# Kernel optimization log

Hardware: AMD Instinct MI355X
Metric: run time of the kernel (lower is better)

The kernel has to match this reference:

```python
import jax, jax.numpy as jnp
import numpy as np

N_QUBITS = 12
FAST_DEPTH = 4
FAST_DECAY = 0.9
LATENT = 512
BATCH = 2048


def _apply_ry(state, theta, wire):
    # state: (B, 2**n) real; RY is a real rotation. PennyLane default.qubit:
    # wire 0 is the most-significant bit of the state index.
    B = state.shape[0]
    s = state.reshape(B, 1 << wire, 2, -1)
    h = theta * 0.5
    c = jnp.cos(h)[:, None, None]
    sn = jnp.sin(h)[:, None, None]
    s0, s1 = s[:, :, 0], s[:, :, 1]
    out = jnp.stack([c * s0 - sn * s1, sn * s0 + c * s1], axis=2)
    return out.reshape(state.shape)


def _apply_cnot_adjacent(state, wire):
    # CNOT with control=wire, target=wire+1 (nearest-neighbor chain)
    B = state.shape[0]
    s = state.reshape(B, 1 << wire, 2, 2, -1)
    out = jnp.stack([s[:, :, 0], s[:, :, 1, ::-1]], axis=2)
    return out.reshape(state.shape)


def _fwp_circuit(x, fast, n_qubits, n_outputs):
    # x: (B, n_qubits) RY encoding angles; fast: (B, depth, n_qubits)
    B = x.shape[0]
    dim = 1 << n_qubits
    # Hadamard layer on |0...0> -> uniform positive real amplitudes.
    state = jnp.full((B, dim), 2.0 ** (-n_qubits / 2), dtype=x.dtype)
    for w in range(n_qubits):
        state = _apply_ry(state, x[:, w], w)
    for layer in range(fast.shape[1]):
        for w in range(n_qubits - 1):
            state = _apply_cnot_adjacent(state, w)
        for w in range(n_qubits):
            state = _apply_ry(state, fast[:, layer, w], w)
    probs = state * state  # real state -> |amp|^2
    outs = []
    for w in range(n_outputs):
        p = probs.reshape(B, 1 << w, 2, -1)
        outs.append(p[:, :, 0].sum(axis=(1, 2)) - p[:, :, 1].sum(axis=(1, 2)))
    return jnp.stack(outs, axis=1)  # (B, n_outputs) PauliZ expvals


def setup_inputs() -> dict:
    key = jax.random.key(0)
    ks = jax.random.split(key, 6)
    n, depth, latent = N_QUBITS, FAST_DEPTH, LATENT
    return {
        "x_t": jax.random.normal(ks[0], (BATCH, n), jnp.float32),
        "fast_prev": jax.random.normal(ks[1], (BATCH, depth, n), jnp.float32) * 0.1,
        "W_enc": jax.random.normal(ks[2], (latent, n), jnp.float32) / np.sqrt(n).astype(np.float32),
        "b_enc": jnp.zeros((latent,), jnp.float32),
        "W_upd": jax.random.normal(ks[3], (depth * n, latent), jnp.float32) / np.sqrt(latent).astype(np.float32),
        "b_upd": jnp.zeros((depth * n,), jnp.float32),
        "W_ro": jax.random.normal(ks[4], (1, n), jnp.float32) / np.sqrt(n).astype(np.float32),
        "b_ro": jnp.zeros((1,), jnp.float32),
    }


def reference(x_t, fast_prev, W_enc, b_enc, W_upd, b_upd, W_ro, b_ro):
    latent = jnp.tanh(x_t @ W_enc.T + b_enc)
    delta = (latent @ W_upd.T + b_upd).reshape(x_t.shape[0], FAST_DEPTH, N_QUBITS)
    fast_next = FAST_DECAY * fast_prev + delta
    q_out = _fwp_circuit(x_t, fast_next, N_QUBITS, N_QUBITS)  # n_outputs = n_qubits
    y_t = q_out @ W_ro.T + b_ro
    return (y_t, fast_next)
```

## Files before the change

### kernel.cpp

```cpp
#include <hip/hip_runtime.h>

static constexpr int NQ    = 12;
static constexpr int DEPTH = 4;
static constexpr int LAT   = 512;
static constexpr int FAST  = DEPTH * NQ;
static constexpr float DECAY = 0.9f;
static constexpr int PITCH = 66;

using v2f = __attribute__((ext_vector_type(2))) float;


#define RAW_FENCE() __threadfence_block()
#define WAR_FENCE() __builtin_amdgcn_wave_barrier()

template<int S>
__device__ __forceinline__ void bfly2(float (&v)[64], float c, float s) {
    v2f c2 = {c, c}, s2 = {s, s};
    #pragma unroll
    for (int r0 = 0; r0 < 64; r0 += 2) {
        if ((r0 & S) == 0) {
            v2f a = {v[r0],     v[r0 + 1]};
            v2f b = {v[r0 + S], v[r0 + S + 1]};
            v2f na = c2 * a - s2 * b;
            v2f nb = s2 * a + c2 * b;
            v[r0]         = na.x;  v[r0 + 1]     = na.y;
            v[r0 + S]     = nb.x;  v[r0 + S + 1] = nb.y;
        }
    }
}

__device__ __forceinline__ void bfly1(float (&v)[64], float c, float s) {
    v2f cs = {c, s}, nsc = {-s, c};
    #pragma unroll
    for (int r0 = 0; r0 < 64; r0 += 2) {
        float a = v[r0], b = v[r0 + 1];
        v2f aa = {a, a}, bb = {b, b};
        v2f res = cs * aa + nsc * bb;
        v[r0]     = res.x;
        v[r0 + 1] = res.y;
    }
}

__device__ __forceinline__ void ry6(float (&v)[64], const float* lc, const float* ls) {
    bfly2<32>(v, lc[0], ls[0]);
    bfly2<16>(v, lc[1], ls[1]);
    bfly2<8>(v, lc[2], ls[2]);
    bfly2<4>(v, lc[3], ls[3]);
    bfly2<2>(v, lc[4], ls[4]);
    bfly1(v, lc[5], ls[5]);
}

__global__ __launch_bounds__(64, 2)
void fwp_kernel(const float* __restrict__ x_t,
                const float* __restrict__ fast_prev,
                const float* __restrict__ W_enc,
                const float* __restrict__ b_enc,
                const float* __restrict__ W_upd,
                const float* __restrict__ b_upd,
                const float* __restrict__ W_ro,
                const float* __restrict__ b_ro,
                float* __restrict__ out_y,
                float* __restrict__ out_fast) {
    const int lane = threadIdx.x;
    const int b    = blockIdx.x;

    __shared__ __align__(16) float s_xch[64 * PITCH];
    __shared__ float s_c[FAST], s_s[FAST];

    float* s_lat = s_xch;

    float xr = (lane < NQ) ? x_t[b * NQ + lane] : 0.0f;
    float xa[NQ];
    #pragma unroll
    for (int k = 0; k < NQ; k++) xa[k] = __shfl(xr, k, 64);

    #pragma unroll
    for (int t = 0; t < LAT / 64; t++) {
        int j = lane + 64 * t;
        const float4* wr = (const float4*)(W_enc + j * NQ);
        float4 a0 = wr[0], a1 = wr[1], a2 = wr[2];
        float sum = b_enc[j]
            + a0.x * xa[0] + a0.y * xa[1] + a0.z * xa[2]  + a0.w * xa[3]
            + a1.x * xa[4] + a1.y * xa[5] + a1.z * xa[6]  + a1.w * xa[7]
            + a2.x * xa[8] + a2.y * xa[9] + a2.z * xa[10] + a2.w * xa[11];
        s_lat[j] = tanhf(sum);
    }
    RAW_FENCE();

    if (lane < FAST) {
        const float4* wr = (const float4*)(W_upd + lane * LAT);
        const float4* lr = (const float4*)(s_lat);
        float sum = b_upd[lane];
        #pragma unroll 16
        for (int j = 0; j < LAT / 4; j++) {
            float4 w4 = wr[j];
            float4 l4 = lr[j];
            sum += w4.x * l4.x + w4.y * l4.y + w4.z * l4.z + w4.w * l4.w;
        }
        float ang = DECAY * fast_prev[b * FAST + lane] + sum;
        out_fast[b * FAST + lane] = ang;
        float hh = 0.5f * ang;
        s_c[lane] = __cosf(hh);
        s_s[lane] = __sinf(hh);
    }
    RAW_FENCE();

    float g0[NQ], g1[NQ];
    #pragma unroll
    for (int w = 0; w < NQ; w++) {
        float hh = 0.5f * xa[w];
        float c = __cosf(hh), s = __sinf(hh);
        g0[w] = (c - s) * 0.70710678118654752f;
        g1[w] = (c + s) * 0.70710678118654752f;
    }
    float L = 1.0f;
    #pragma unroll
    for (int w = 0; w < 6; w++)
        L *= ((lane >> (5 - w)) & 1) ? g1[w] : g0[w];

    float v[64];
    v[0] = L;
    #pragma unroll
    for (int w = 6; w < NQ; w++) {
        const int S = 1 << (11 - w);
        #pragma unroll
        for (int r = 0; r < 64; r += 2 * S) {
            v[r + S] = v[r] * g1[w];
            v[r]     = v[r] * g0[w];
        }
    }

    const int A0 = ((lane ^ (lane >> 1)) & 31) | (lane & 32);
    const int A1 = A0 ^ 32;

    #pragma unroll
    for (int layer = 0; layer < DEPTH; layer++) {
        float lc[NQ], ls[NQ];
        #pragma unroll
        for (int w = 0; w < NQ; w++) {
            lc[w] = s_c[layer * NQ + w];
            ls[w] = s_s[layer * NQ + w];
        }

        WAR_FENCE();
        #pragma unroll
        for (int k = 0; k < 32; k++)
            *(v2f*)&s_xch[lane * PITCH + 2 * k] = (v2f){v[2 * k], v[2 * k + 1]};
        RAW_FENCE();
        #pragma unroll
        for (int r = 0; r < 64; r++) {
            const int g = r ^ (r >> 1);
            v[r] = s_xch[g * PITCH + ((r & 1) ? A1 : A0)];
        }
        ry6(v, lc, ls);

        WAR_FENCE();
        #pragma unroll
        for (int k = 0; k < 32; k++)
            *(v2f*)&s_xch[lane * PITCH + 2 * k] = (v2f){v[2 * k], v[2 * k + 1]};
        RAW_FENCE();
        #pragma unroll
        for (int r = 0; r < 64; r++) v[r] = s_xch[r * PITCH + lane];
        ry6(v, lc + 6, ls + 6);
    }

    float tot = 0.0f, pw[6] = {0, 0, 0, 0, 0, 0};
    #pragma unroll
    for (int r = 0; r < 64; r++) {
        float p = v[r] * v[r];
        tot += p;
        pw[0] += (r & 32) ? -p : p;
        pw[1] += (r & 16) ? -p : p;
        pw[2] += (r & 8)  ? -p : p;
        pw[3] += (r & 4)  ? -p : p;
        pw[4] += (r & 2)  ? -p : p;
        pw[5] += (r & 1)  ? -p : p;
    }
    float sl = 0.0f;
    #pragma unroll
    for (int w = 0; w < 6; w++) {
        float c = W_ro[w];
        sl += ((lane >> (5 - w)) & 1) ? -c : c;
    }
    float y = sl * tot;
    #pragma unroll
    for (int k = 0; k < 6; k++) y += W_ro[6 + k] * pw[k];
    #pragma unroll
    for (int m = 32; m >= 1; m >>= 1) y += __shfl_xor(y, m, 64);
    if (lane == 0) out_y[b] = y + b_ro[0];
}

extern "C" void kernel_launch(void* const* d_in, const int* in_sizes, int n_in,
                              void* d_out, int out_size, void* d_ws, size_t ws_size,
                              hipStream_t stream) {
    const float* x_t       = (const float*)d_in[0];
    const float* fast_prev = (const float*)d_in[1];
    const float* W_enc     = (const float*)d_in[2];
    const float* b_enc     = (const float*)d_in[3];
    const float* W_upd     = (const float*)d_in[4];
    const float* b_upd     = (const float*)d_in[5];
    const float* W_ro      = (const float*)d_in[6];
    const float* b_ro      = (const float*)d_in[7];
    float* out = (float*)d_out;

    fwp_kernel<<<2048, 64, 0, stream>>>(x_t, fast_prev, W_enc, b_enc,
                                        W_upd, b_upd, W_ro, b_ro,
                                        out , out + 2048 );
}
```

Measured before the change: 111.3 us.

## Split butterfly stages into halves to overlap LDS reads and drop fences

Each 6-wire RY block becomes two 5-wire butterfly passes over the 32-element halves plus a final stride-32 butterfly. The second half of the LDS transpose reads can then be issued while the first half is still being rotated. All block fences and wave barriers around the shared-memory exchange are removed, since the block is a single 64-lane wavefront. The x row is also read directly from global memory by every lane instead of being broadcast with shuffles. Without fences, correct ordering of the LDS exchange now depends on the compiler not reordering accesses across lanes.

```diff
diff --git a/kernel.cpp b/kernel.cpp
--- a/kernel.cpp
+++ b/kernel.cpp
@@ -10,14 +10,11 @@
 using v2f = __attribute__((ext_vector_type(2))) float;
 
 
-#define RAW_FENCE() __threadfence_block()
-#define WAR_FENCE() __builtin_amdgcn_wave_barrier()
-
-template<int S>
-__device__ __forceinline__ void bfly2(float (&v)[64], float c, float s) {
+template<int S, int B>
+__device__ __forceinline__ void bfly_half(float (&v)[64], float c, float s) {
     v2f c2 = {c, c}, s2 = {s, s};
     #pragma unroll
-    for (int r0 = 0; r0 < 64; r0 += 2) {
+    for (int r0 = B; r0 < B + 32; r0 += 2) {
         if ((r0 & S) == 0) {
             v2f a = {v[r0],     v[r0 + 1]};
             v2f b = {v[r0 + S], v[r0 + S + 1]};
@@ -29,10 +26,11 @@
     }
 }
 
-__device__ __forceinline__ void bfly1(float (&v)[64], float c, float s) {
+template<int B>
+__device__ __forceinline__ void bfly1_half(float (&v)[64], float c, float s) {
     v2f cs = {c, s}, nsc = {-s, c};
     #pragma unroll
-    for (int r0 = 0; r0 < 64; r0 += 2) {
+    for (int r0 = B; r0 < B + 32; r0 += 2) {
         float a = v[r0], b = v[r0 + 1];
         v2f aa = {a, a}, bb = {b, b};
         v2f res = cs * aa + nsc * bb;
@@ -41,13 +39,26 @@
     }
 }
 
-__device__ __forceinline__ void ry6(float (&v)[64], const float* lc, const float* ls) {
-    bfly2<32>(v, lc[0], ls[0]);
-    bfly2<16>(v, lc[1], ls[1]);
-    bfly2<8>(v, lc[2], ls[2]);
-    bfly2<4>(v, lc[3], ls[3]);
-    bfly2<2>(v, lc[4], ls[4]);
-    bfly1(v, lc[5], ls[5]);
+template<int B>
+__device__ __forceinline__ void ry5_half(float (&v)[64], const float* c, const float* s) {
+    bfly_half<16, B>(v, c[0], s[0]);
+    bfly_half<8,  B>(v, c[1], s[1]);
+    bfly_half<4,  B>(v, c[2], s[2]);
+    bfly_half<2,  B>(v, c[3], s[3]);
+    bfly1_half<B>(v, c[4], s[4]);
+}
+
+__device__ __forceinline__ void bfly32(float (&v)[64], float c, float s) {
+    v2f c2 = {c, c}, s2 = {s, s};
+    #pragma unroll
+    for (int r0 = 0; r0 < 32; r0 += 2) {
+        v2f a = {v[r0],      v[r0 + 1]};
+        v2f b = {v[r0 + 32], v[r0 + 33]};
+        v2f na = c2 * a - s2 * b;
+        v2f nb = s2 * a + c2 * b;
+        v[r0]      = na.x;  v[r0 + 1]  = na.y;
+        v[r0 + 32] = nb.x;  v[r0 + 33] = nb.y;
+    }
 }
 
 __global__ __launch_bounds__(64, 2)
@@ -69,10 +80,10 @@
 
     float* s_lat = s_xch;
 
-    float xr = (lane < NQ) ? x_t[b * NQ + lane] : 0.0f;
+    const float* xrow = x_t + b * NQ;
     float xa[NQ];
     #pragma unroll
-    for (int k = 0; k < NQ; k++) xa[k] = __shfl(xr, k, 64);
+    for (int k = 0; k < NQ; k++) xa[k] = xrow[k];
 
     #pragma unroll
     for (int t = 0; t < LAT / 64; t++) {
@@ -85,7 +96,6 @@
             + a2.x * xa[8] + a2.y * xa[9] + a2.z * xa[10] + a2.w * xa[11];
         s_lat[j] = tanhf(sum);
     }
-    RAW_FENCE();
 
     if (lane < FAST) {
         const float4* wr = (const float4*)(W_upd + lane * LAT);
@@ -103,7 +113,6 @@
         s_c[lane] = __cosf(hh);
         s_s[lane] = __sinf(hh);
     }
-    RAW_FENCE();
 
     float g0[NQ], g1[NQ];
     #pragma unroll
@@ -142,26 +151,33 @@
             ls[w] = s_s[layer * NQ + w];
         }
 
-        WAR_FENCE();
         #pragma unroll
         for (int k = 0; k < 32; k++)
             *(v2f*)&s_xch[lane * PITCH + 2 * k] = (v2f){v[2 * k], v[2 * k + 1]};
-        RAW_FENCE();
-        #pragma unroll
-        for (int r = 0; r < 64; r++) {
+        #pragma unroll
+        for (int r = 0; r < 32; r++) {
             const int g = r ^ (r >> 1);
             v[r] = s_xch[g * PITCH + ((r & 1) ? A1 : A0)];
         }
-        ry6(v, lc, ls);
-
-        WAR_FENCE();
+        ry5_half<0>(v, lc + 1, ls + 1);
+        #pragma unroll
+        for (int r = 32; r < 64; r++) {
+            const int g = r ^ (r >> 1);
+            v[r] = s_xch[g * PITCH + ((r & 1) ? A1 : A0)];
+        }
+        ry5_half<32>(v, lc + 1, ls + 1);
+        bfly32(v, lc[0], ls[0]);
+
         #pragma unroll
         for (int k = 0; k < 32; k++)
             *(v2f*)&s_xch[lane * PITCH + 2 * k] = (v2f){v[2 * k], v[2 * k + 1]};
-        RAW_FENCE();
-        #pragma unroll
-        for (int r = 0; r < 64; r++) v[r] = s_xch[r * PITCH + lane];
-        ry6(v, lc + 6, ls + 6);
+        #pragma unroll
+        for (int r = 0; r < 32; r++) v[r] = s_xch[r * PITCH + lane];
+        ry5_half<0>(v, lc + 7, ls + 7);
+        #pragma unroll
+        for (int r = 32; r < 64; r++) v[r] = s_xch[r * PITCH + lane];
+        ry5_half<32>(v, lc + 7, ls + 7);
+        bfly32(v, lc[6], ls[6]);
     }
 
     float tot = 0.0f, pw[6] = {0, 0, 0, 0, 0, 0};
```

Measured after the change: 111.8 us. About the same (+0.5%).
